# Kernel optimization log

Measured on AMD Instinct MI355X. Metric: run time of the kernel, lower is better.

The kernel has to match this reference:

```python
import jax, jax.numpy as jnp
import numpy as np

DIM = 1024
HEADS = 8


def setup_inputs() -> dict:
    key = jax.random.key(0)
    ks = jax.random.split(key, 8)
    b, n, m, nc, d = 2, 1024, 4, 1024, DIM
    x = jax.random.normal(ks[0], (b, n, d), dtype=jnp.float32)
    context = jax.random.normal(ks[1], (b, m, nc, d), dtype=jnp.float32)
    doc_similarities = jax.random.normal(ks[2], (b, m), dtype=jnp.float32)
    # learned params (Linear weights stored as [in, out] for x @ W)
    s = 1.0 / np.sqrt(d)
    Wq = jax.random.uniform(ks[3], (d, d), minval=-s, maxval=s, dtype=jnp.float32)
    Wkv = jax.random.uniform(ks[4], (d, 2 * d), minval=-s, maxval=s, dtype=jnp.float32)
    Wout = jax.random.uniform(ks[5], (d, d), minval=-s, maxval=s, dtype=jnp.float32)
    bout = jax.random.uniform(ks[6], (d,), minval=-s, maxval=s, dtype=jnp.float32)
    beta = jnp.array(1.0, dtype=jnp.float32)
    return {"x": x, "context": context, "doc_similarities": doc_similarities,
            "Wq": Wq, "Wkv": Wkv, "beta": beta, "Wout": Wout, "bout": bout}


def reference(x, context, doc_similarities, Wq, Wkv, beta, Wout, bout):
    b, n, dim = x.shape
    h = HEADS
    hd = dim // h
    scale = dim ** -0.5
    m, nc = context.shape[1], context.shape[2]

    # q: [b, h, n, hd]
    q = (x @ Wq).reshape(b, n, h, hd).transpose(0, 2, 1, 3)

    # flatten docs: [b, m*nc, dim]
    ctx = context.reshape(b, m * nc, dim)
    # doc similarity bias, repeated per token within each doc: [b, m*nc]
    sim = jnp.repeat(doc_similarities, nc, axis=1) * beta

    kv = ctx @ Wkv  # [b, L, 2*dim]
    k, v = jnp.split(kv, 2, axis=-1)
    k = k.reshape(b, m * nc, h, hd).transpose(0, 2, 1, 3)  # [b, h, L, hd]
    v = v.reshape(b, m * nc, h, hd).transpose(0, 2, 1, 3)

    dots = jnp.einsum('bhid,bhjd->bhij', q, k) * scale
    dots = dots + sim[:, None, None, :]
    attn = jax.nn.softmax(dots, axis=-1)
    out = jnp.einsum('bhij,bhjd->bhid', attn, v)
    out = out.transpose(0, 2, 1, 3).reshape(b, n, dim)
    return out @ Wout + bout
```

## Files before the change

kernel.cpp:

```cpp
#include <hip/hip_runtime.h>
#include <stdint.h>

typedef __attribute__((ext_vector_type(4))) float f32x4;
typedef __attribute__((ext_vector_type(8))) __bf16 bf16x8;

__device__ __forceinline__ uint16_t f2bf(float f) {
  uint32_t u = __builtin_bit_cast(uint32_t, f);
  u += 0x7FFFu + ((u >> 16) & 1u);
  return (uint16_t)(u >> 16);
}

__device__ __forceinline__ float bf2f(uint16_t u) {
  uint32_t v = ((uint32_t)u) << 16;
  return __builtin_bit_cast(float, v);
}

__device__ __forceinline__ void load_lds16(const uint16_t* g, uint16_t* l) {
  __builtin_amdgcn_global_load_lds((const __attribute__((address_space(1))) void*)g,
                                   (__attribute__((address_space(3))) void*)l, 16, 0, 0);
}

__global__ __launch_bounds__(256) void k_prep(const float* __restrict__ x,
                                              const float* __restrict__ ctx,
                                              const float* __restrict__ Wq,
                                              const float* __restrict__ Wkv,
                                              const float* __restrict__ Wout,
                                              uint16_t* __restrict__ xb,
                                              uint16_t* __restrict__ ctxb,
                                              uint16_t* __restrict__ wqt,
                                              uint16_t* __restrict__ wkvt,
                                              uint16_t* __restrict__ woutt,
                                              float qscale) {
  __shared__ float tile[32][33];
  int id = blockIdx.x;
  int tid = threadIdx.x;
  if (id < 10240) {
    const float* in;
    uint16_t* out;
    int j = id * 256 + tid;
    if (j < 524288) { in = x; out = xb; }
    else            { in = ctx; out = ctxb; j -= 524288; }
    float4 v = ((const float4*)in)[j];
    union { uint16_t u[4]; uint64_t q; } o;
    o.u[0] = f2bf(v.x); o.u[1] = f2bf(v.y); o.u[2] = f2bf(v.z); o.u[3] = f2bf(v.w);
    ((uint64_t*)out)[j] = o.q;
    return;
  }
  id -= 10240;
  const float* W;
  uint16_t* Wt;
  int N, n0, k0;
  float sc = 1.0f;
  if (id < 1024)      { W = Wq;   Wt = wqt;   N = 1024; sc = qscale;
                        n0 = (id & 31) * 32; k0 = (id >> 5) * 32; }
  else if (id < 2048) { W = Wout; Wt = woutt; N = 1024; id -= 1024;
                        n0 = (id & 31) * 32; k0 = (id >> 5) * 32; }
  else                { W = Wkv;  Wt = wkvt;  N = 2048; id -= 2048;
                        n0 = (id & 63) * 32; k0 = (id >> 6) * 32; }
  int c = tid & 31, r0 = tid >> 5;
#pragma unroll
  for (int i = 0; i < 4; i++) {
    int r = r0 + i * 8;
    tile[r][c] = W[(size_t)(k0 + r) * N + n0 + c];
  }
  __syncthreads();
#pragma unroll
  for (int i = 0; i < 4; i++) {
    int r = r0 + i * 8;
    Wt[(size_t)(n0 + r) * 1024 + k0 + c] = f2bf(tile[c][r] * sc);
  }
}

__global__ __launch_bounds__(256) void k_gemm_fused(const uint16_t* __restrict__ ctxb,
                                                    const uint16_t* __restrict__ wkvt,
                                                    const uint16_t* __restrict__ xb,
                                                    const uint16_t* __restrict__ wqt,
                                                    uint16_t* __restrict__ kb,
                                                    uint16_t* __restrict__ vtb,
                                                    uint16_t* __restrict__ qb) {
  __shared__ uint16_t smem[9216];
  uint16_t* la = smem;
  uint16_t* lb = smem + 4096;
  const int K = 1024;
  const int tid = threadIdx.x;
  const int lane = tid & 63, w = tid >> 6;
  const int quad = lane >> 4, l16 = lane & 15;
  const int wr = (w >> 1) * 64, wc = (w & 1) * 64;
  int id = blockIdx.x;
  int bx, by, isQ;
  const uint16_t *Ab, *Bb;
  if (id < 1024) {
    isQ = 0; bx = id & 15; by = id >> 4;
    Ab = ctxb + (size_t)by * 128 * K;
    Bb = wkvt + (size_t)bx * 128 * K;
  } else {
    isQ = 1; id -= 1024; bx = id & 7; by = id >> 3;
    Ab = xb + (size_t)by * 128 * K;
    Bb = wqt + (size_t)bx * 128 * K;
  }
  f32x4 acc[4][4] = {};
  const int rA = tid >> 2, slotA = tid & 3;
  const int rA1 = rA + 64;
  const int segA0 = (slotA ^ ((rA + (rA >> 2)) & 3)) * 8;
  const int segA1 = (slotA ^ ((rA1 + (rA1 >> 2)) & 3)) * 8;
  for (int k0 = 0; k0 < K; k0 += 32) {
    __syncthreads();
    load_lds16(Ab + (size_t)rA * K + k0 + segA0, la + tid * 8);
    load_lds16(Ab + (size_t)rA1 * K + k0 + segA1, la + (tid + 256) * 8);
    load_lds16(Bb + (size_t)rA * K + k0 + segA0, lb + tid * 8);
    load_lds16(Bb + (size_t)rA1 * K + k0 + segA1, lb + (tid + 256) * 8);
    __syncthreads();
    bf16x8 af[4], bfr[4];
#pragma unroll
    for (int i = 0; i < 4; i++) {
      int R = wr + i * 16 + l16;
      int s = quad ^ ((R + (R >> 2)) & 3);
      af[i] = *(const bf16x8*)&la[R * 32 + s * 8];
    }
#pragma unroll
    for (int j = 0; j < 4; j++) {
      int R = wc + j * 16 + l16;
      int s = quad ^ ((R + (R >> 2)) & 3);
      bfr[j] = *(const bf16x8*)&lb[R * 32 + s * 8];
    }
#pragma unroll
    for (int i = 0; i < 4; i++)
#pragma unroll
      for (int j = 0; j < 4; j++)
        acc[i][j] = __builtin_amdgcn_mfma_f32_16x16x32_bf16(af[i], bfr[j], acc[i][j], 0, 0, 0);
  }
  __syncthreads();
  if (isQ) {
#pragma unroll
    for (int i = 0; i < 4; i++)
#pragma unroll
      for (int j = 0; j < 4; j++) {
        size_t row = (size_t)by * 128 + wr + i * 16 + quad * 4;
        size_t col = (size_t)bx * 128 + wc + j * 16 + l16;
#pragma unroll
        for (int r = 0; r < 4; r++)
          qb[(row + r) * 1024 + col] = f2bf(acc[i][j][r]);
      }
  } else if (bx < 8) {
#pragma unroll
    for (int i = 0; i < 4; i++)
#pragma unroll
      for (int j = 0; j < 4; j++) {
        size_t row = (size_t)by * 128 + wr + i * 16 + quad * 4;
        size_t col = (size_t)bx * 128 + wc + j * 16 + l16;
#pragma unroll
        for (int r = 0; r < 4; r++)
          kb[(row + r) * 1024 + col] = f2bf(acc[i][j][r]);
      }
  } else {
    const int bh = (by >> 5) * 8 + (bx - 8);
    const int lbase = (by & 31) * 128;
    uint16_t* vdst = vtb + (size_t)bh * 524288;
#pragma unroll
    for (int half = 0; half < 2; half++) {
      if (wr == half * 64) {
#pragma unroll
        for (int i = 0; i < 4; i++)
#pragma unroll
          for (int j = 0; j < 4; j++) {
            int rowl = i * 16 + quad * 4;
            int col = wc + j * 16 + l16;
            union { uint64_t q; uint16_t u[4]; } pk;
#pragma unroll
            for (int r = 0; r < 4; r++) pk.u[r] = f2bf(acc[i][j][r]);
            *(uint64_t*)&smem[col * 72 + rowl] = pk.q;
          }
      }
      __syncthreads();
      {
        int col = tid >> 1, rseg = (tid & 1) * 32;
        const uint16_t* src = &smem[col * 72 + rseg];
        uint16_t* d = vdst + (size_t)col * 4096 + lbase + half * 64 + rseg;
#pragma unroll
        for (int k = 0; k < 4; k++)
          ((uint4*)d)[k] = *(const uint4*)&src[k * 8];
      }
      __syncthreads();
    }
  }
}

__global__ __launch_bounds__(256) void k_gemm64(const uint16_t* __restrict__ A,
                                                const uint16_t* __restrict__ Bt,
                                                float* __restrict__ Cf,
                                                const float* __restrict__ bias,
                                                int M, int N, int K) {
  __shared__ uint16_t la[64 * 64];
  __shared__ uint16_t lb[64 * 64];
  const int tid = threadIdx.x;
  const int lane = tid & 63, w = tid >> 6;
  const int quad = lane >> 4, l16 = lane & 15;
  const int wr = (w >> 1) * 32, wc = (w & 1) * 32;
  const size_t tr0 = (size_t)blockIdx.y * 64, tc0 = (size_t)blockIdx.x * 64;
  f32x4 acc[2][2] = {};
  const int rS = tid >> 3, sS = tid & 7;
  const int seg = (sS ^ (rS & 7)) * 8;
  const uint16_t* Ab = A + tr0 * K;
  const uint16_t* Bb = Bt + tc0 * K;
  for (int k0 = 0; k0 < K; k0 += 64) {
    __syncthreads();
    load_lds16(Ab + (size_t)rS * K + k0 + seg, la + tid * 8);
    load_lds16(Ab + (size_t)(rS + 32) * K + k0 + seg, la + (tid + 256) * 8);
    load_lds16(Bb + (size_t)rS * K + k0 + seg, lb + tid * 8);
    load_lds16(Bb + (size_t)(rS + 32) * K + k0 + seg, lb + (tid + 256) * 8);
    __syncthreads();
#pragma unroll
    for (int sub = 0; sub < 2; sub++) {
      const int kk = sub * 4 + quad;
      bf16x8 af[2], bfr[2];
#pragma unroll
      for (int i = 0; i < 2; i++) {
        int R = wr + i * 16 + l16;
        af[i] = *(const bf16x8*)&la[R * 64 + (kk ^ (R & 7)) * 8];
      }
#pragma unroll
      for (int j = 0; j < 2; j++) {
        int R = wc + j * 16 + l16;
        bfr[j] = *(const bf16x8*)&lb[R * 64 + (kk ^ (R & 7)) * 8];
      }
#pragma unroll
      for (int i = 0; i < 2; i++)
#pragma unroll
        for (int j = 0; j < 2; j++)
          acc[i][j] = __builtin_amdgcn_mfma_f32_16x16x32_bf16(af[i], bfr[j], acc[i][j], 0, 0, 0);
    }
  }
#pragma unroll
  for (int i = 0; i < 2; i++) {
#pragma unroll
    for (int j = 0; j < 2; j++) {
      size_t row = tr0 + wr + i * 16 + quad * 4;
      size_t col = tc0 + wc + j * 16 + l16;
#pragma unroll
      for (int r = 0; r < 4; r++)
        Cf[(row + r) * N + col] = acc[i][j][r] + bias[col];
    }
  }
}

__global__ __launch_bounds__(256) void k_attn(const uint16_t* __restrict__ q,
                                              const uint16_t* __restrict__ kb,
                                              const uint16_t* __restrict__ vt,
                                              const float* __restrict__ sims,
                                              const float* __restrict__ beta,
                                              uint16_t* __restrict__ po,
                                              float* __restrict__ pl) {
  __shared__ uint16_t Kl[8192];
  __shared__ uint16_t Vl[8192];
  __shared__ uint16_t Pl[4096];
  const int idx = blockIdx.x;
  const int qbx = idx >> 7, g = idx & 127;
  const int h = g >> 4, b = (g >> 3) & 1, sp = g & 7;
  const int q0 = qbx * 128;
  const int tid = threadIdx.x, lane = tid & 63, w = tid >> 6;
  const int quad = lane >> 4, l16 = lane & 15;
  const float wsplit =
      __builtin_amdgcn_exp2f(sims[b * 4 + (sp >> 1)] * beta[0] * 1.44269504f);
  uint16_t* Pw = Pl + w * 1024;

  union { uint32_t u[4]; bf16x8 v; } Oc;
#pragma unroll
  for (int j = 0; j < 4; j++) Oc.u[j] = 0x3F803F80u;
  const bf16x8 onesf = Oc.v;

  bf16x8 qf[2][4];
#pragma unroll
  for (int rb = 0; rb < 2; rb++) {
    const uint16_t* qrow =
        q + ((size_t)(b * 1024 + q0 + w * 32 + rb * 16 + l16)) * 1024 + h * 128 + quad * 8;
#pragma unroll
    for (int ks = 0; ks < 4; ks++) qf[rb][ks] = *(const bf16x8*)(qrow + ks * 32);
  }
  f32x4 o[2][8] = {};
  f32x4 o9[2] = {};

  const uint16_t* kptr = kb + ((size_t)(b * 4096 + sp * 512)) * 1024 + h * 128;
  const uint16_t* vptr = vt + ((size_t)(b * 8 + h) * 128) * 4096 + sp * 512;

  for (int c = 0; c < 8; c++) {
    __syncthreads();
#pragma unroll
    for (int ii = 0; ii < 4; ii++) {
      int g2 = tid + ii * 256;
      int row = g2 >> 4, seg = (g2 & 15) ^ (row & 15);
      load_lds16(kptr + (size_t)row * 1024 + seg * 8, Kl + g2 * 8);
    }
#pragma unroll
    for (int ii = 0; ii < 4; ii++) {
      int g2 = tid + ii * 256;
      int row = g2 >> 3, seg = (g2 & 7) ^ (row & 7);
      load_lds16(vptr + (size_t)row * 4096 + seg * 8, Vl + g2 * 8);
    }
    __syncthreads();
#pragma unroll
    for (int kh = 0; kh < 2; kh++) {
#pragma unroll
      for (int nb2 = 0; nb2 < 2; nb2++) {
        const int nb = kh * 2 + nb2;
        f32x4 s0 = {}, s1 = {};
#pragma unroll
        for (int ks = 0; ks < 4; ks++) {
          bf16x8 kf = *(const bf16x8*)&Kl[(nb * 16 + l16) * 128 + (((ks * 4 + quad) ^ l16) * 8)];
          s0 = __builtin_amdgcn_mfma_f32_16x16x32_bf16(qf[0][ks], kf, s0, 0, 0, 0);
          s1 = __builtin_amdgcn_mfma_f32_16x16x32_bf16(qf[1][ks], kf, s1, 0, 0, 0);
        }
        const int sl = nb2 * 2 + (l16 >> 3);
#pragma unroll
        for (int r = 0; r < 4; r++) {
          int rp0 = quad * 4 + r;
          Pw[rp0 * 32 + ((sl ^ ((rp0 >> 1) & 3)) * 8) + (l16 & 7)] =
              f2bf(__builtin_amdgcn_exp2f(s0[r]));
          int rp1 = 16 + rp0;
          Pw[rp1 * 32 + ((sl ^ ((rp1 >> 1) & 3)) * 8) + (l16 & 7)] =
              f2bf(__builtin_amdgcn_exp2f(s1[r]));
        }
      }
      __asm__ volatile("s_waitcnt lgkmcnt(0)" ::: "memory");
      const int segp = (quad ^ ((l16 >> 1) & 3)) * 8;
      bf16x8 pf0 = *(const bf16x8*)&Pw[l16 * 32 + segp];
      bf16x8 pf1 = *(const bf16x8*)&Pw[(16 + l16) * 32 + segp];
      const int sq = ((kh * 4 + quad) ^ (l16 & 7)) * 8;
#pragma unroll
      for (int nb = 0; nb < 8; nb++) {
        bf16x8 vf = *(const bf16x8*)&Vl[(nb * 16 + l16) * 64 + sq];
        o[0][nb] = __builtin_amdgcn_mfma_f32_16x16x32_bf16(pf0, vf, o[0][nb], 0, 0, 0);
        o[1][nb] = __builtin_amdgcn_mfma_f32_16x16x32_bf16(pf1, vf, o[1][nb], 0, 0, 0);
      }
      o9[0] = __builtin_amdgcn_mfma_f32_16x16x32_bf16(pf0, onesf, o9[0], 0, 0, 0);
      o9[1] = __builtin_amdgcn_mfma_f32_16x16x32_bf16(pf1, onesf, o9[1], 0, 0, 0);
    }
    kptr += (size_t)64 * 1024;
    vptr += 64;
  }
  const int rowbase = (sp * 16 + b * 8 + h) * 1024 + q0 + w * 32;
#pragma unroll
  for (int rb = 0; rb < 2; rb++)
#pragma unroll
    for (int r = 0; r < 4; r++) {
      int row = rowbase + rb * 16 + quad * 4 + r;
#pragma unroll
      for (int nb = 0; nb < 8; nb++)
        po[(size_t)row * 128 + nb * 16 + l16] = f2bf(o[rb][nb][r] * wsplit);
      if (l16 == 0)
        pl[row] = o9[rb][r] * wsplit;
    }
}

__global__ __launch_bounds__(256) void k_merge(const uint16_t* __restrict__ po,
                                               const float* __restrict__ pl,
                                               uint16_t* __restrict__ attb) {
  const int bq = blockIdx.x;
  const int b = bq >> 10, qi = bq & 1023;
  const int t = threadIdx.x;
  const int h = t >> 5, d0 = (t & 31) * 4;
  const int bh = b * 8 + h;
  float den = 0.f;
  float acc[4] = {0.f, 0.f, 0.f, 0.f};
#pragma unroll
  for (int s = 0; s < 8; s++) {
    den += pl[(s * 16 + bh) * 1024 + qi];
    union { uint64_t q; uint16_t u[4]; } v;
    v.q = *(const uint64_t*)&po[(((size_t)(s * 16 + bh)) * 1024 + qi) * 128 + d0];
#pragma unroll
    for (int j = 0; j < 4; j++) acc[j] += bf2f(v.u[j]);
  }
  const float inv = 1.0f / den;
  union { uint64_t q; uint16_t u[4]; } o;
#pragma unroll
  for (int j = 0; j < 4; j++) o.u[j] = f2bf(acc[j] * inv);
  *(uint64_t*)&attb[((size_t)(b * 1024 + qi)) * 1024 + h * 128 + d0] = o.q;
}

extern "C" void kernel_launch(void* const* d_in, const int* in_sizes, int n_in,
                              void* d_out, int out_size, void* d_ws, size_t ws_size,
                              hipStream_t stream) {
  (void)in_sizes; (void)n_in; (void)out_size; (void)ws_size;
  const float* x    = (const float*)d_in[0];
  const float* ctx  = (const float*)d_in[1];
  const float* sims = (const float*)d_in[2];
  const float* Wq   = (const float*)d_in[3];
  const float* Wkv  = (const float*)d_in[4];
  const float* beta = (const float*)d_in[5];
  const float* Wout = (const float*)d_in[6];
  const float* bout = (const float*)d_in[7];
  float* out = (float*)d_out;

  char* ws = (char*)d_ws;
  uint16_t* xb    = (uint16_t*)(ws + 0);
  uint16_t* ctxb  = (uint16_t*)(ws + (4u << 20));
  uint16_t* wqt   = (uint16_t*)(ws + (20u << 20));
  uint16_t* wkvt  = (uint16_t*)(ws + (22u << 20));
  uint16_t* kb    = (uint16_t*)(ws + (32u << 20));
  uint16_t* vtb   = (uint16_t*)(ws + (48u << 20));
  float*    pl    = (float*)   (ws + (64u << 20));
  uint16_t* woutt = (uint16_t*)(ws + (68u << 20));
  uint16_t* qb    = (uint16_t*)(ws + (70u << 20));
  uint16_t* attb  = (uint16_t*)(ws + (74u << 20));
  uint16_t* po = (uint16_t*)(ws + 0);

  const float LOG2E = 1.44269504f;
  const float qscale = 0.03125f * LOG2E;

  k_prep<<<14336, 256, 0, stream>>>(x, ctx, Wq, Wkv, Wout, xb, ctxb, wqt, wkvt, woutt, qscale);
  k_gemm_fused<<<1152, 256, 0, stream>>>(ctxb, wkvt, xb, wqt, kb, vtb, qb);
  k_attn<<<1024, 256, 0, stream>>>(qb, kb, vtb, sims, beta, po, pl);
  k_merge<<<2048, 256, 0, stream>>>(po, pl, attb);
  k_gemm64<<<dim3(16, 32), 256, 0, stream>>>(attb, woutt, out, bout, 2048, 1024, 1024);
}
```

Before: 231.9 us.

## Widen GEMM K-tile, remap blocks per XCD, fuse split-K merge into attention

The fused QKV GEMM now stages 64-wide K tiles with an 8-way XOR swizzle, halving the number of barrier pairs per block. Block indices are also remapped so that tiles sharing A rows land on the same XCD, aiming for better L2 reuse. The separate merge kernel is removed: each attention block bumps an atomic counter, and the last of the 8 splits reduces the partial outputs into attb. This saves a launch and some traffic, at the cost of a memset, threadfences, and a serialized reduction tail done by one block per group.

```diff
diff --git a/kernel.cpp b/kernel.cpp
--- a/kernel.cpp
+++ b/kernel.cpp
@@ -78,9 +78,9 @@
                                                     uint16_t* __restrict__ kb,
                                                     uint16_t* __restrict__ vtb,
                                                     uint16_t* __restrict__ qb) {
-  __shared__ uint16_t smem[9216];
+  __shared__ uint16_t smem[16384];
   uint16_t* la = smem;
-  uint16_t* lb = smem + 4096;
+  uint16_t* lb = smem + 8192;
   const int K = 1024;
   const int tid = threadIdx.x;
   const int lane = tid & 63, w = tid >> 6;
@@ -90,44 +90,51 @@
   int bx, by, isQ;
   const uint16_t *Ab, *Bb;
   if (id < 1024) {
-    isQ = 0; bx = id & 15; by = id >> 4;
+    isQ = 0;
+    int xcd = id & 7, t = id >> 3;
+    by = (xcd << 3) + (t & 7);
+    bx = t >> 3;
     Ab = ctxb + (size_t)by * 128 * K;
     Bb = wkvt + (size_t)bx * 128 * K;
   } else {
-    isQ = 1; id -= 1024; bx = id & 7; by = id >> 3;
+    isQ = 1; id -= 1024;
+    int xcd = id & 7, t = id >> 3;
+    by = (xcd << 1) + (t & 1);
+    bx = t >> 1;
     Ab = xb + (size_t)by * 128 * K;
     Bb = wqt + (size_t)bx * 128 * K;
   }
   f32x4 acc[4][4] = {};
-  const int rA = tid >> 2, slotA = tid & 3;
-  const int rA1 = rA + 64;
-  const int segA0 = (slotA ^ ((rA + (rA >> 2)) & 3)) * 8;
-  const int segA1 = (slotA ^ ((rA1 + (rA1 >> 2)) & 3)) * 8;
-  for (int k0 = 0; k0 < K; k0 += 32) {
-    __syncthreads();
-    load_lds16(Ab + (size_t)rA * K + k0 + segA0, la + tid * 8);
-    load_lds16(Ab + (size_t)rA1 * K + k0 + segA1, la + (tid + 256) * 8);
-    load_lds16(Bb + (size_t)rA * K + k0 + segA0, lb + tid * 8);
-    load_lds16(Bb + (size_t)rA1 * K + k0 + segA1, lb + (tid + 256) * 8);
-    __syncthreads();
-    bf16x8 af[4], bfr[4];
-#pragma unroll
-    for (int i = 0; i < 4; i++) {
-      int R = wr + i * 16 + l16;
-      int s = quad ^ ((R + (R >> 2)) & 3);
-      af[i] = *(const bf16x8*)&la[R * 32 + s * 8];
-    }
-#pragma unroll
-    for (int j = 0; j < 4; j++) {
-      int R = wc + j * 16 + l16;
-      int s = quad ^ ((R + (R >> 2)) & 3);
-      bfr[j] = *(const bf16x8*)&lb[R * 32 + s * 8];
-    }
-#pragma unroll
-    for (int i = 0; i < 4; i++)
-#pragma unroll
-      for (int j = 0; j < 4; j++)
-        acc[i][j] = __builtin_amdgcn_mfma_f32_16x16x32_bf16(af[i], bfr[j], acc[i][j], 0, 0, 0);
+  for (int k0 = 0; k0 < K; k0 += 64) {
+    __syncthreads();
+#pragma unroll
+    for (int ii = 0; ii < 4; ii++) {
+      int g = tid + ii * 256;
+      int row = g >> 3, slot = g & 7, seg = (slot ^ (row & 7)) * 8;
+      load_lds16(Ab + (size_t)row * K + k0 + seg, la + g * 8);
+      load_lds16(Bb + (size_t)row * K + k0 + seg, lb + g * 8);
+    }
+    __syncthreads();
+#pragma unroll
+    for (int sub = 0; sub < 2; sub++) {
+      const int kk = sub * 4 + quad;
+      bf16x8 af[4], bfr[4];
+#pragma unroll
+      for (int i = 0; i < 4; i++) {
+        int R = wr + i * 16 + l16;
+        af[i] = *(const bf16x8*)&la[R * 64 + ((kk ^ (R & 7)) * 8)];
+      }
+#pragma unroll
+      for (int j = 0; j < 4; j++) {
+        int R = wc + j * 16 + l16;
+        bfr[j] = *(const bf16x8*)&lb[R * 64 + ((kk ^ (R & 7)) * 8)];
+      }
+#pragma unroll
+      for (int i = 0; i < 4; i++)
+#pragma unroll
+        for (int j = 0; j < 4; j++)
+          acc[i][j] = __builtin_amdgcn_mfma_f32_16x16x32_bf16(af[i], bfr[j], acc[i][j], 0, 0, 0);
+    }
   }
   __syncthreads();
   if (isQ) {
@@ -249,10 +256,13 @@
                                               const float* __restrict__ sims,
                                               const float* __restrict__ beta,
                                               uint16_t* __restrict__ po,
-                                              float* __restrict__ pl) {
+                                              float* __restrict__ pl,
+                                              uint32_t* __restrict__ cnt,
+                                              uint16_t* __restrict__ attb) {
   __shared__ uint16_t Kl[8192];
   __shared__ uint16_t Vl[8192];
   __shared__ uint16_t Pl[4096];
+  __shared__ int isLast;
   const int idx = blockIdx.x;
   const int qbx = idx >> 7, g = idx & 127;
   const int h = g >> 4, b = (g >> 3) & 1, sp = g & 7;
@@ -349,31 +359,41 @@
       if (l16 == 0)
         pl[row] = o9[rb][r] * wsplit;
     }
-}
-
-__global__ __launch_bounds__(256) void k_merge(const uint16_t* __restrict__ po,
-                                               const float* __restrict__ pl,
-                                               uint16_t* __restrict__ attb) {
-  const int bq = blockIdx.x;
-  const int b = bq >> 10, qi = bq & 1023;
-  const int t = threadIdx.x;
-  const int h = t >> 5, d0 = (t & 31) * 4;
+  __threadfence();
+  if (tid == 0) {
+    const int grp = (qbx << 4) + (g >> 3);
+    isLast = (atomicAdd(&cnt[grp], 1u) == 7u) ? 1 : 0;
+  }
+  __syncthreads();
+  if (!isLast) return;
+  __threadfence();
   const int bh = b * 8 + h;
+  const int qi = q0 + (tid >> 1);
+  const int d0 = (tid & 1) * 64;
   float den = 0.f;
-  float acc[4] = {0.f, 0.f, 0.f, 0.f};
-#pragma unroll
-  for (int s = 0; s < 8; s++) {
-    den += pl[(s * 16 + bh) * 1024 + qi];
-    union { uint64_t q; uint16_t u[4]; } v;
-    v.q = *(const uint64_t*)&po[(((size_t)(s * 16 + bh)) * 1024 + qi) * 128 + d0];
-#pragma unroll
-    for (int j = 0; j < 4; j++) acc[j] += bf2f(v.u[j]);
-  }
+#pragma unroll
+  for (int s = 0; s < 8; s++) den += pl[(s * 16 + bh) * 1024 + qi];
   const float inv = 1.0f / den;
-  union { uint64_t q; uint16_t u[4]; } o;
-#pragma unroll
-  for (int j = 0; j < 4; j++) o.u[j] = f2bf(acc[j] * inv);
-  *(uint64_t*)&attb[((size_t)(b * 1024 + qi)) * 1024 + h * 128 + d0] = o.q;
+#pragma unroll
+  for (int p = 0; p < 4; p++) {
+    float acc[16] = {};
+#pragma unroll
+    for (int s = 0; s < 8; s++) {
+      const uint16_t* src =
+          po + ((size_t)((s * 16 + bh) * 1024 + qi)) * 128 + d0 + p * 16;
+      union { uint4 v; uint16_t u[8]; } a0, a1;
+      a0.v = *(const uint4*)src;
+      a1.v = *(const uint4*)(src + 8);
+#pragma unroll
+      for (int j = 0; j < 8; j++) { acc[j] += bf2f(a0.u[j]); acc[8 + j] += bf2f(a1.u[j]); }
+    }
+    union { uint4 v[2]; uint16_t u[16]; } ov;
+#pragma unroll
+    for (int j = 0; j < 16; j++) ov.u[j] = f2bf(acc[j] * inv);
+    uint16_t* dst = attb + ((size_t)(b * 1024 + qi)) * 1024 + h * 128 + d0 + p * 16;
+    *(uint4*)dst = ov.v[0];
+    *(uint4*)(dst + 8) = ov.v[1];
+  }
 }
 
 extern "C" void kernel_launch(void* const* d_in, const int* in_sizes, int n_in,
@@ -398,17 +418,18 @@
   uint16_t* kb    = (uint16_t*)(ws + (32u << 20));
   uint16_t* vtb   = (uint16_t*)(ws + (48u << 20));
   float*    pl    = (float*)   (ws + (64u << 20));
+  uint32_t* cnt   = (uint32_t*)(ws + (65u << 20));
   uint16_t* woutt = (uint16_t*)(ws + (68u << 20));
   uint16_t* qb    = (uint16_t*)(ws + (70u << 20));
   uint16_t* attb  = (uint16_t*)(ws + (74u << 20));
-  uint16_t* po = (uint16_t*)(ws + 0);
+  uint16_t* po    = (uint16_t*)(ws + 0);
 
   const float LOG2E = 1.44269504f;
   const float qscale = 0.03125f * LOG2E;
 
+  hipMemsetAsync(cnt, 0, 128 * sizeof(uint32_t), stream);
   k_prep<<<14336, 256, 0, stream>>>(x, ctx, Wq, Wkv, Wout, xb, ctxb, wqt, wkvt, woutt, qscale);
   k_gemm_fused<<<1152, 256, 0, stream>>>(ctxb, wkvt, xb, wqt, kb, vtb, qb);
-  k_attn<<<1024, 256, 0, stream>>>(qb, kb, vtb, sims, beta, po, pl);
-  k_merge<<<2048, 256, 0, stream>>>(po, pl, attb);
+  k_attn<<<1024, 256, 0, stream>>>(qb, kb, vtb, sims, beta, po, pl, cnt, attb);
   k_gemm64<<<dim3(16, 32), 256, 0, stream>>>(attb, woutt, out, bout, 2048, 1024, 1024);
 }
```

After: 496.2 us. 114% more time.
